# Kernel tuning notes

Hardware: AMD Instinct MI355X
Metric: run time of the kernel (lower is better)

## Reference

```python
import jax, jax.numpy as jnp
import numpy as np
import math

EMBED_DIM = 512
NUM_HEADS = 8
NUM_EXPERTS = 16
TOP_K = 8
B, T = 2, 1024


def setup_inputs() -> dict:
    key = jax.random.key(0)
    ks = jax.random.split(key, 16)
    d, E = EMBED_DIM, NUM_EXPERTS
    hdim = 4 * d  # expert hidden width
    s = 0.02
    inp = {
        "x": jax.random.normal(ks[0], (B, T, d), jnp.float32),
        # RMSNorm params (init ones, matching torch module)
        "g": jnp.ones((d,), jnp.float32),
        "b": jnp.ones((d,), jnp.float32),
        # attention
        "c_attn_w": jax.random.normal(ks[1], (d, 3 * d), jnp.float32) * s,
        "c_attn_b": jnp.zeros((3 * d,), jnp.float32),
        "alpha": jnp.ones((NUM_HEADS,), jnp.float32),
        "c_proj_w": jax.random.normal(ks[2], (d, d), jnp.float32) * s,
        "c_proj_b": jnp.zeros((d,), jnp.float32),
        # router
        "router_w": jax.random.normal(ks[3], (d, E), jnp.float32) * s,
        "router_b": jnp.zeros((E,), jnp.float32),
        # stacked expert params: Linear(d,4d) -> SwiGLU(4d,4d) -> Linear(4d,d)
        "w_in": jax.random.normal(ks[4], (E, d, hdim), jnp.float32) * s,
        "b_in": jnp.zeros((E, hdim), jnp.float32),
        "w1": jax.random.normal(ks[5], (E, hdim, 2 * hdim), jnp.float32) * s,
        "b1": jnp.zeros((E, 2 * hdim), jnp.float32),
        "w2": jax.random.normal(ks[6], (E, hdim, hdim), jnp.float32) * s,
        "b2": jnp.zeros((E, hdim), jnp.float32),
        "w_out": jax.random.normal(ks[7], (E, hdim, d), jnp.float32) * s,
        "b_out": jnp.zeros((E, d), jnp.float32),
    }
    return inp


def _block(x, g, b, c_attn_w, c_attn_b, alpha, c_proj_w, c_proj_b,
           router_w, router_b, w_in, b_in, w1, b1, w2, b2, w_out, b_out):
    Bb, Tt, C = x.shape
    H = alpha.shape[0]
    hd = C // H
    E = router_b.shape[0]

    # RMSNorm (note: additive b, per original module)
    rms = jnp.sqrt(jnp.mean(x * x, axis=-1, keepdims=True) + 1e-6)
    xn = (x / rms) * g + b

    # QK-normalized causal attention
    qkv = xn @ c_attn_w + c_attn_b                      # [B,T,3C]
    q, k, v = jnp.split(qkv, 3, axis=-1)
    def heads(t):
        return t.reshape(Bb, Tt, H, hd).transpose(0, 2, 1, 3)  # [B,H,T,hd]
    q, k, v = heads(q), heads(k), heads(v)
    eps = 1e-5
    q_hat = q / (jnp.linalg.norm(q, axis=-1, keepdims=True) + eps)
    k_hat = k / (jnp.linalg.norm(k, axis=-1, keepdims=True) + eps)
    factor = (alpha * math.sqrt(hd)).reshape(1, H, 1, 1)
    q_scaled = q_hat * factor
    # SDPA default scale = 1/sqrt(head_dim)
    scores = jnp.einsum("bhqd,bhkd->bhqk", q_scaled, k_hat) / math.sqrt(hd)
    causal = jnp.tril(jnp.ones((Tt, Tt), bool))
    scores = jnp.where(causal, scores, -jnp.inf)
    att = jax.nn.softmax(scores, axis=-1)
    y = jnp.einsum("bhqk,bhkd->bhqd", att, v)
    y = y.transpose(0, 2, 1, 3).reshape(Bb, Tt, C)
    y = y @ c_proj_w + c_proj_b
    x = x + y

    # Router + top-8 normalized gates
    routes = jax.nn.softmax(x @ router_w + router_b, axis=-1)  # [B,T,E]
    probs, idx = jax.lax.top_k(routes, TOP_K)
    probs = probs / jnp.sum(probs, axis=-1, keepdims=True)
    # combine weights per expert: [B,T,E]
    gates = jnp.sum(jax.nn.one_hot(idx, E, dtype=x.dtype) * probs[..., None], axis=2)

    # Dense expert evaluation (faithful math: unselected tokens get zero gate)
    N = Bb * Tt
    xf = x.reshape(N, C)
    gf = gates.reshape(N, E)
    h = jnp.einsum("nd,edf->enf", xf, w_in) + b_in[:, None, :]      # [E,N,4d]
    c = jnp.einsum("enf,efg->eng", h, w1) + b1[:, None, :]          # [E,N,8d]
    a, bb2 = jnp.split(c, 2, axis=-1)
    s = (bb2 * jax.nn.sigmoid(bb2)) * a                              # SwiGLU
    o = jnp.einsum("enf,efg->eng", s, w2) + b2[:, None, :]          # [E,N,4d]
    eo = jnp.einsum("enf,efd->end", o, w_out) + b_out[:, None, :]   # [E,N,d]
    moe = jnp.einsum("end,ne->nd", eo, gf).reshape(Bb, Tt, C)
    return x + moe


def reference(x, g, b, c_attn_w, c_attn_b, alpha, c_proj_w, c_proj_b,
              router_w, router_b, w_in, b_in, w1, b1, w2, b2, w_out, b_out):
    return _block(x, g, b, c_attn_w, c_attn_b, alpha, c_proj_w, c_proj_b,
                  router_w, router_b, w_in, b_in, w1, b1, w2, b2, w_out, b_out)
```

## Files before the change

kernel.cpp:

```cpp
#include <hip/hip_runtime.h>
#include <stdint.h>

#define DEVI __device__ __forceinline__
#define FENCE() asm volatile("" ::: "memory")
#define BAR() do{ FENCE(); __builtin_amdgcn_s_barrier(); FENCE(); }while(0)

typedef short short8 __attribute__((ext_vector_type(8)));
typedef short short4v __attribute__((ext_vector_type(4)));
typedef float f32x4 __attribute__((ext_vector_type(4)));

DEVI float bf2f(unsigned short s){ union{unsigned u; float f;} x; x.u = ((unsigned)s)<<16; return x.f; }
DEVI unsigned short f2bf(float f){ union{float f; unsigned u;} x; x.f=f; unsigned r = x.u + 0x7fff + ((x.u>>16)&1); return (unsigned short)(r>>16); }

DEVI void gload_lds16(const void* g, void* l){
  __builtin_amdgcn_global_load_lds((const __attribute__((address_space(1))) unsigned int*)g,
                                   (__attribute__((address_space(3))) unsigned int*)l, 16, 0, 0);
}

__global__ __launch_bounds__(256)
void transpose_cvt(const float* __restrict__ in, unsigned short* __restrict__ out, int K, int N)
{
  __shared__ float tile[32][33];
  size_t zoff = (size_t)blockIdx.z * K * N;
  const float* src = in + zoff;
  unsigned short* dst = out + zoff;
  int kb = blockIdx.y*32, nb = blockIdx.x*32;
  int t = threadIdx.x;
  int tr = t>>3, tc = (t&7)*4;
  float4 v = *(const float4*)(src + (size_t)(kb+tr)*N + nb + tc);
  tile[tr][tc+0]=v.x; tile[tr][tc+1]=v.y; tile[tr][tc+2]=v.z; tile[tr][tc+3]=v.w;
  __syncthreads();
  short4v ov;
  ov[0] = (short)f2bf(tile[tc+0][tr]);
  ov[1] = (short)f2bf(tile[tc+1][tr]);
  ov[2] = (short)f2bf(tile[tc+2][tr]);
  ov[3] = (short)f2bf(tile[tc+3][tr]);
  *(short4v*)(dst + (size_t)(nb+tr)*K + kb + tc) = ov;
}

__global__ __launch_bounds__(256)
void transpose_cvt_w1(const float* __restrict__ w1, unsigned short* __restrict__ outp)
{
  __shared__ float tile[32][33];
  int e = blockIdx.z;
  const float* src = w1 + (size_t)e*2048*4096;
  unsigned short* dst = outp + (size_t)e*4096*2048;
  int np0 = blockIdx.x*32;
  int k0 = blockIdx.y*32;
  int g = np0 >> 5;
  int t = threadIdx.x;
  int tr = t>>3, tc = (t&7)*4;
  int srccol = (tc < 16) ? (g*16 + tc) : (2048 + g*16 + (tc-16));
  float4 v = *(const float4*)(src + (size_t)(k0+tr)*4096 + srccol);
  tile[tr][tc+0]=v.x; tile[tr][tc+1]=v.y; tile[tr][tc+2]=v.z; tile[tr][tc+3]=v.w;
  __syncthreads();
  short4v ov;
  ov[0] = (short)f2bf(tile[tc+0][tr]);
  ov[1] = (short)f2bf(tile[tc+1][tr]);
  ov[2] = (short)f2bf(tile[tc+2][tr]);
  ov[3] = (short)f2bf(tile[tc+3][tr]);
  *(short4v*)(dst + (size_t)(np0+tr)*2048 + k0 + tc) = ov;
}

__global__ __launch_bounds__(256)
void rmsnorm_k(const float* __restrict__ x, const float* __restrict__ gw,
               const float* __restrict__ bw, unsigned short* __restrict__ xn)
{
  int row = blockIdx.x*4 + (threadIdx.x>>6);
  int lane = threadIdx.x & 63;
  const float* xr = x + (size_t)row*512 + lane*8;
  float4 a = *(const float4*)xr;
  float4 c = *(const float4*)(xr+4);
  float ss = a.x*a.x+a.y*a.y+a.z*a.z+a.w*a.w + c.x*c.x+c.y*c.y+c.z*c.z+c.w*c.w;
  #pragma unroll
  for (int m=1;m<64;m<<=1) ss += __shfl_xor(ss, m);
  float inv = 1.0f / sqrtf(ss*(1.f/512.f) + 1e-6f);
  const float* gr = gw + lane*8; const float* br = bw + lane*8;
  float4 g0=*(const float4*)gr, g1=*(const float4*)(gr+4);
  float4 b0=*(const float4*)br, b1=*(const float4*)(br+4);
  short8 o;
  o[0]=(short)f2bf(a.x*inv*g0.x + b0.x);
  o[1]=(short)f2bf(a.y*inv*g0.y + b0.y);
  o[2]=(short)f2bf(a.z*inv*g0.z + b0.z);
  o[3]=(short)f2bf(a.w*inv*g0.w + b0.w);
  o[4]=(short)f2bf(c.x*inv*g1.x + b1.x);
  o[5]=(short)f2bf(c.y*inv*g1.y + b1.y);
  o[6]=(short)f2bf(c.z*inv*g1.z + b1.z);
  o[7]=(short)f2bf(c.w*inv*g1.w + b1.w);
  *(short8*)(xn + (size_t)row*512 + lane*8) = o;
}

#define READ_AFR(Q) do{ \
  _Pragma("unroll") \
  for (int m2=0;m2<2;m2++){ \
    int rt = wm*128 + ((Q)*2+m2)*16 + lrow; \
    _Pragma("unroll") \
    for (int kk=0;kk<2;kk++) \
      afr[m2][kk] = *(const short8*)(sA + rt*128 + (((lg+kk*4)^(rt&7))<<4)); \
  } \
}while(0)

#define QUADP(Q) do{ \
  __builtin_amdgcn_s_setprio(1); \
  _Pragma("unroll") \
  for (int m2=0;m2<2;m2++){ \
    _Pragma("unroll") \
    for (int n=0;n<4;n++){ \
      _Pragma("unroll") \
      for (int kk=0;kk<2;kk++) \
        acc[(Q)*2+m2][n] = __builtin_amdgcn_mfma_f32_16x16x32_bf16(afr[m2][kk], bfr[n][kk], acc[(Q)*2+m2][n], 0,0,0); \
    } \
  } \
  __builtin_amdgcn_s_setprio(0); \
}while(0)

template<int EPI>
__global__ __launch_bounds__(512, 2)
void gemmT(const unsigned short* __restrict__ A, const unsigned short* __restrict__ B,
           const float* __restrict__ bias,
           float* __restrict__ Cf, unsigned short* __restrict__ Ch,
           int M, int N, int K,
           const int* __restrict__ off, long long strideBz, long long strideBiasz)
{
  __shared__ char smem[131072];
  int z = blockIdx.z;
  int rowbase = 0, Mz = M;
  if (off){ rowbase = off[z]; Mz = off[z+1] - rowbase; }
  int row0 = blockIdx.y * 256;
  if (row0 >= Mz) return;
  int col0 = blockIdx.x * 256;
  const unsigned short* Ab = A + (size_t)(rowbase + row0) * K;
  const unsigned short* Bb = B + (size_t)z * strideBz + (size_t)col0 * K;
  const float* biasz = bias + (size_t)z * strideBiasz;

  int tid = threadIdx.x;
  int lane = tid & 63, w = tid >> 6;
  int lrow = lane & 15, lg = lane >> 4;
  int wm = w >> 2, wn = w & 3;

  f32x4 acc[8][4];
  #pragma unroll
  for (int i=0;i<8;i++){
    #pragma unroll
    for (int j=0;j<4;j++) acc[i][j] = f32x4{0.f,0.f,0.f,0.f};
  }
  int nkt = K >> 6;
  auto stage = [&](int kt2, int H){
    if (kt2 >= nkt) return;
    char* sl = smem + (kt2 & 1) * 65536 + H * 16384;
    int k0 = kt2 << 6;
    const unsigned short* src = (H < 2) ? Ab : Bb;
    int rbase = (H & 1) * 128;
    #pragma unroll
    for (int i=0;i<2;i++){
      int si = i*512 + tid;
      int r = si >> 3, kb = (si & 7) ^ (r & 7);
      gload_lds16(src + (size_t)(rbase + r)*K + k0 + kb*8, sl + si*16);
    }
  };
  stage(0,0); stage(0,1); stage(0,2); stage(0,3);
  stage(1,2); stage(1,3);
  asm volatile("s_waitcnt vmcnt(4)" ::: "memory");
  BAR();
  for (int kt = 0; kt < nkt; kt++){
    char* sA = smem + (kt & 1) * 65536;
    char* sB = sA + 32768;
    short8 bfr[4][2], afr[2][2];
    #pragma unroll
    for (int n=0;n<4;n++){
      int ct = wn*64 + n*16 + lrow;
      #pragma unroll
      for (int kk=0;kk<2;kk++)
        bfr[n][kk] = *(const short8*)(sB + ct*128 + (((lg+kk*4)^(ct&7))<<4));
    }
    READ_AFR(0);
    stage(kt+1, 0); stage(kt+1, 1);
    BAR();
    QUADP(0);
    BAR();
    READ_AFR(1);
    stage(kt+2, 2);
    BAR();
    QUADP(1);
    BAR();
    READ_AFR(2);
    stage(kt+2, 3);
    BAR();
    QUADP(2);
    BAR();
    READ_AFR(3);
    if (kt + 2 < nkt) { asm volatile("s_waitcnt vmcnt(4)" ::: "memory"); }
    else              { asm volatile("s_waitcnt vmcnt(0)" ::: "memory"); }
    BAR();
    QUADP(3);
    BAR();
  }
  #pragma unroll
  for (int m=0;m<8;m++){
    #pragma unroll
    for (int j=0;j<4;j++){
      int row = row0 + wm*128 + m*16 + lg*4 + j;
      if (row < Mz){
        size_t rg = (size_t)(rowbase + row);
        if constexpr (EPI == 2){
          #pragma unroll
          for (int nf=0;nf<4;nf+=2){
            int pcol = col0 + wn*64 + nf*16;
            int scol = ((pcol>>5)<<4) + lrow;
            float av = acc[m][nf][j]   + biasz[scol];
            float gv = acc[m][nf+1][j] + biasz[2048 + scol];
            float sg = gv / (1.f + __expf(-gv));
            Ch[rg*2048 + scol] = f2bf(av * sg);
          }
        } else {
          #pragma unroll
          for (int n=0;n<4;n++){
            int col = col0 + wn*64 + n*16 + lrow;
            float v = acc[m][n][j] + biasz[col];
            size_t idx = rg * N + col;
            if constexpr (EPI == 0) Cf[idx] = v;
            else                    Ch[idx] = f2bf(v);
          }
        }
      }
    }
  }
}

__global__ __launch_bounds__(256)
void gemm_proj(const unsigned short* __restrict__ A, const unsigned short* __restrict__ B,
               const float* __restrict__ bias,
               float* __restrict__ Cf, unsigned short* __restrict__ Ch,
               const float* __restrict__ resid, int M, int N, int K)
{
  __shared__ char smem[32768];
  char* smA = smem; char* smB = smem + 16384;
  int row0 = blockIdx.y * 128;
  int col0 = blockIdx.x * 128;
  int t = threadIdx.x, w = t>>6, lane = t&63;
  int lrow = lane&15, lg = lane>>4;
  int wr = w>>1, wc = w&1;

  f32x4 acc[4][4];
  #pragma unroll
  for (int i=0;i<4;i++){
    #pragma unroll
    for (int j=0;j<4;j++) acc[i][j] = f32x4{0.f,0.f,0.f,0.f};
  }
  const size_t Abase = (size_t)row0 * K;
  const size_t Bbase = (size_t)col0 * K;
  int nkt = K >> 6;
  for (int kt=0; kt<nkt; kt++){
    __syncthreads();
    int k0 = kt*64;
    #pragma unroll
    for (int i=0;i<4;i++){
      int s = (i*4 + w)*64 + lane;
      int r = s>>3;
      int kb = (s&7) ^ (r&7);
      gload_lds16(A + Abase + (size_t)r*K + k0 + kb*8, smA + (size_t)(i*4+w)*1024);
      gload_lds16(B + Bbase + (size_t)r*K + k0 + kb*8, smB + (size_t)(i*4+w)*1024);
    }
    __syncthreads();
    #pragma unroll
    for (int ks=0; ks<2; ks++){
      short8 af[4], bf[4];
      int kbb = lg + ks*4;
      #pragma unroll
      for (int m=0;m<4;m++){
        int rt = wr*64 + m*16 + lrow;
        af[m] = *(const short8*)(smA + rt*128 + ((kbb ^ (rt&7))<<4));
      }
      #pragma unroll
      for (int n=0;n<4;n++){
        int rt = wc*64 + n*16 + lrow;
        bf[n] = *(const short8*)(smB + rt*128 + ((kbb ^ (rt&7))<<4));
      }
      #pragma unroll
      for (int m=0;m<4;m++){
        #pragma unroll
        for (int n=0;n<4;n++)
          acc[m][n] = __builtin_amdgcn_mfma_f32_16x16x32_bf16(af[m], bf[n], acc[m][n], 0,0,0);
      }
    }
  }
  #pragma unroll
  for (int m=0;m<4;m++){
    int rloc = wr*64 + m*16 + lg*4;
    #pragma unroll
    for (int j=0;j<4;j++){
      int row = row0 + rloc + j;
      size_t rg = (size_t)row;
      #pragma unroll
      for (int n=0;n<4;n++){
        int col = col0 + wc*64 + n*16 + lrow;
        float v = acc[m][n][j] + bias[col];
        size_t idx = rg * N + col;
        v += resid[idx];
        Cf[idx] = v;
        Ch[idx] = f2bf(v);
      }
    }
  }
}

__global__ __launch_bounds__(256)
void prep_qkv(const float* __restrict__ qkv, const float* __restrict__ alpha,
              unsigned short* __restrict__ q_s, unsigned short* __restrict__ k_hat,
              unsigned short* __restrict__ v_t)
{
  int idx = blockIdx.x*4 + (threadIdx.x>>6);
  int lane = threadIdx.x & 63;
  int h = idx & 7, bt = idx >> 3;
  size_t base = (size_t)bt*1536 + h*64 + lane;
  float qv = qkv[base], kv = qkv[base+512], vv = qkv[base+1024];
  float qs2 = qv*qv, ks2 = kv*kv;
  #pragma unroll
  for (int m=1;m<64;m<<=1){ qs2 += __shfl_xor(qs2, m); ks2 += __shfl_xor(ks2, m); }
  float qh = qv / (sqrtf(qs2) + 1e-5f) * alpha[h];
  float kh = kv / (sqrtf(ks2) + 1e-5f);
  int b = bt >> 10, tt = bt & 1023;
  size_t hb = ((size_t)(b*8+h))*1024*64;
  q_s[hb + (size_t)tt*64 + lane] = f2bf(qh);
  k_hat[hb + (size_t)tt*64 + lane] = f2bf(kh);
  v_t[((size_t)(b*8+h)*64 + lane)*1024 + tt] = f2bf(vv);
}

__global__ __launch_bounds__(256)
void attn_k(const unsigned short* __restrict__ q_s, const unsigned short* __restrict__ k_hat,
            const unsigned short* __restrict__ v_t, unsigned short* __restrict__ y)
{
  __shared__ char sm[51200];
  char* smK = sm + 18432;
  char* smV = sm + 34816;
  int qt = blockIdx.x, bh = blockIdx.y;
  int b = bh>>3, h = bh&7;
  int t = threadIdx.x, w = t>>6, lane = t&63;
  int lrow = lane&15, lg = lane>>4;
  int q0 = qt*64;
  const size_t hQK = (size_t)bh*1024*64;
  const size_t hV  = (size_t)bh*64*1024;

  #pragma unroll
  for (int i=0;i<2;i++){
    int si = i*256 + t;
    int r = si>>3, kb = (si&7)^(r&7);
    gload_lds16(q_s + hQK + (size_t)(q0+r)*64 + kb*8, sm + (size_t)si*16);
  }
  __syncthreads();
  short8 qf[2];
  #pragma unroll
  for (int ks=0;ks<2;ks++){
    int rt = w*16 + lrow;
    int kbb = lg + ks*4;
    qf[ks] = *(const short8*)(sm + rt*128 + ((kbb^(rt&7))<<4));
  }
  f32x4 oacc[4];
  #pragma unroll
  for (int j=0;j<4;j++) oacc[j] = f32x4{0.f,0.f,0.f,0.f};
  float mrun[4], lrun[4];
  #pragma unroll
  for (int j=0;j<4;j++){ mrun[j] = -1e30f; lrun[j] = 0.f; }
  char* Pw = sm + w*2304;

  int ktmax = (q0 + 63) >> 7;
  for (int kt=0; kt<=ktmax; kt++){
    __syncthreads();
    int t0 = kt*128;
    #pragma unroll
    for (int i=0;i<4;i++){
      int s = (i*4+w)*64 + lane;
      int r = s>>3, kb = (s&7)^(r&7);
      gload_lds16(k_hat + hQK + (size_t)(t0+r)*64 + kb*8, smK + (size_t)(i*4+w)*1024);
    }
    #pragma unroll
    for (int i=0;i<4;i++){
      int s = (i*4+w)*64 + lane;
      int d = s>>4, kb2 = s&15;
      int kb = kb2 ^ (d&7);
      gload_lds16(v_t + hV + (size_t)d*1024 + t0 + kb*8, smV + (size_t)(i*4+w)*1024);
    }
    __syncthreads();

    f32x4 sacc[8];
    #pragma unroll
    for (int j=0;j<8;j++) sacc[j] = f32x4{0.f,0.f,0.f,0.f};
    #pragma unroll
    for (int ks=0;ks<2;ks++){
      short8 kf[8];
      int kbb = lg + ks*4;
      #pragma unroll
      for (int nf=0;nf<8;nf++){
        int rt = nf*16+lrow;
        kf[nf] = *(const short8*)(smK + rt*128 + ((kbb^(rt&7))<<4));
      }
      #pragma unroll
      for (int nf=0;nf<8;nf++)
        sacc[nf] = __builtin_amdgcn_mfma_f32_16x16x32_bf16(qf[ks], kf[nf], sacc[nf], 0,0,0);
    }
    if (kt == ktmax){
      #pragma unroll
      for (int nf=0;nf<8;nf++){
        #pragma unroll
        for (int j=0;j<4;j++){
          int qi = q0 + w*16 + lg*4 + j;
          int ki = t0 + nf*16 + lrow;
          if (ki > qi) sacc[nf][j] = -1e30f;
        }
      }
    }
    #pragma unroll
    for (int j=0;j<4;j++){
      float mx = sacc[0][j];
      #pragma unroll
      for (int nf=1;nf<8;nf++) mx = fmaxf(mx, sacc[nf][j]);
      #pragma unroll
      for (int m=1;m<16;m<<=1) mx = fmaxf(mx, __shfl_xor(mx, m));
      float mnew = fmaxf(mrun[j], mx);
      float sc = __expf(mrun[j] - mnew);
      float rs = 0.f;
      #pragma unroll
      for (int nf=0;nf<8;nf++){
        float p = __expf(sacc[nf][j] - mnew);
        sacc[nf][j] = p; rs += p;
      }
      #pragma unroll
      for (int m=1;m<16;m<<=1) rs += __shfl_xor(rs, m);
      lrun[j] = lrun[j]*sc + rs;
      mrun[j] = mnew;
      #pragma unroll
      for (int n2=0;n2<4;n2++) oacc[n2][j] *= sc;
    }
    #pragma unroll
    for (int half=0; half<2; half++){
      #pragma unroll
      for (int nfh=0;nfh<4;nfh++){
        int nf = half*4 + nfh;
        #pragma unroll
        for (int j=0;j<4;j++){
          int row = lg*4 + j;
          int col = nfh*16 + lrow;
          *(unsigned short*)(Pw + (row*72 + col)*2) = f2bf(sacc[nf][j]);
        }
      }
      #pragma unroll
      for (int k2=0;k2<2;k2++){
        int ks2 = half*2 + k2;
        short8 pf, vf[4];
        pf = *(const short8*)(Pw + lrow*144 + lg*16 + k2*64);
        #pragma unroll
        for (int n2=0;n2<4;n2++){
          int d = n2*16+lrow;
          int kbb2 = lg + ks2*4;
          vf[n2] = *(const short8*)(smV + d*256 + ((kbb2^(d&7))<<4));
        }
        #pragma unroll
        for (int n2=0;n2<4;n2++)
          oacc[n2] = __builtin_amdgcn_mfma_f32_16x16x32_bf16(pf, vf[n2], oacc[n2], 0,0,0);
      }
    }
  }
  #pragma unroll
  for (int n2=0;n2<4;n2++){
    #pragma unroll
    for (int j=0;j<4;j++){
      float v = oacc[n2][j] / lrun[j];
      int qi = q0 + w*16 + lg*4 + j;
      int d = n2*16 + lrow;
      y[((size_t)(b*1024+qi))*512 + h*64 + d] = f2bf(v);
    }
  }
}

__global__ __launch_bounds__(256)
void router_topk(const float* __restrict__ x2f, const float* __restrict__ rw,
                 const float* __restrict__ rb, float* __restrict__ gates)
{
  int tkn = blockIdx.x*4 + (threadIdx.x>>6);
  int lane = threadIdx.x & 63;
  int e = lane & 15, p = lane >> 4;
  const float* xr = x2f + (size_t)tkn*512;
  float part = 0.f;
  for (int d = p*128; d < p*128+128; d++)
    part += xr[d] * rw[d*16 + e];
  part += __shfl_xor(part, 16);
  part += __shfl_xor(part, 32);
  float logit = part + rb[e];
  float mx = logit;
  #pragma unroll
  for (int m=1;m<16;m<<=1) mx = fmaxf(mx, __shfl_xor(mx, m));
  float ex = __expf(logit - mx);
  float sm = ex;
  #pragma unroll
  for (int m=1;m<16;m<<=1) sm += __shfl_xor(sm, m);
  float prob = ex / sm;
  bool taken = false;
  float ssum = 0.f;
  #pragma unroll
  for (int r=0;r<8;r++){
    float cv = taken ? -1.f : prob;
    int ci = e;
    #pragma unroll
    for (int m=1;m<16;m<<=1){
      float ov = __shfl_xor(cv, m);
      int oi = __shfl_xor(ci, m);
      if (ov > cv || (ov == cv && oi < ci)){ cv = ov; ci = oi; }
    }
    if (e == ci) taken = true;
    ssum += cv;
  }
  if (lane < 16)
    gates[(size_t)tkn*16 + e] = taken ? prob / ssum : 0.f;
}

__global__ void listbuild(const float* __restrict__ gates, int* __restrict__ list,
                          int* __restrict__ slot, int* __restrict__ cnt)
{
  int e = blockIdx.x;
  int tid = threadIdx.x, w = tid>>6, lane = tid&63;
  __shared__ int sbase;
  __shared__ int wsum[4];
  if (tid==0) sbase = 0;
  __syncthreads();
  for (int c=0;c<8;c++){
    int tk = c*256 + tid;
    bool flag = gates[(size_t)tk*16 + e] > 0.f;
    unsigned long long bal = __ballot(flag);
    if (lane==0) wsum[w] = (int)__popcll(bal);
    __syncthreads();
    int wpref = 0;
    for (int i=0;i<w;i++) wpref += wsum[i];
    int tot = wsum[0]+wsum[1]+wsum[2]+wsum[3];
    int lpref = (int)__popcll(bal & ((1ull<<lane)-1ull));
    if (flag){
      int pos = sbase + wpref + lpref;
      list[e*2048 + pos] = tk;
      slot[(size_t)tk*16 + e] = pos;
    }
    __syncthreads();
    if (tid==0) sbase += tot;
    __syncthreads();
  }
  if (tid==0) cnt[e] = sbase;
}

__global__ void prefix_off(const int* __restrict__ cnt, int* __restrict__ off){
  if (threadIdx.x==0 && blockIdx.x==0){
    int a=0;
    for (int e=0;e<16;e++){ off[e]=a; a+=cnt[e]; }
    off[16]=a;
  }
}

__global__ __launch_bounds__(256)
void gather_rows(const unsigned short* __restrict__ x2h, const int* __restrict__ list,
                 const int* __restrict__ cnt, const int* __restrict__ off,
                 unsigned short* __restrict__ xe)
{
  int e = blockIdx.y;
  int s = blockIdx.x*4 + (threadIdx.x>>6);
  if (s >= cnt[e]) return;
  int lane = threadIdx.x & 63;
  int tk = list[e*2048 + s];
  *(short8*)(xe + ((size_t)(off[e]+s))*512 + lane*8) =
      *(const short8*)(x2h + (size_t)tk*512 + lane*8);
}

__global__ __launch_bounds__(256)
void combine_k(const float* __restrict__ x2f, const unsigned short* __restrict__ eo,
               const float* __restrict__ gates, const int* __restrict__ slot,
               const int* __restrict__ off, float* __restrict__ out)
{
  int tkn = blockIdx.x;
  __shared__ float gs[16];
  __shared__ int rws[16];
  int tid = threadIdx.x;
  if (tid < 16){
    float g = gates[(size_t)tkn*16 + tid];
    gs[tid] = g;
    rws[tid] = (g > 0.f) ? (off[tid] + slot[(size_t)tkn*16 + tid]) : 0;
  }
  __syncthreads();
  for (int d = tid; d < 512; d += 256){
    float v = x2f[(size_t)tkn*512 + d];
    #pragma unroll
    for (int e=0;e<16;e++){
      float g = gs[e];
      if (g > 0.f) v += g * bf2f(eo[(size_t)rws[e]*512 + d]);
    }
    out[(size_t)tkn*512 + d] = v;
  }
}

extern "C" void kernel_launch(void* const* d_in, const int* in_sizes, int n_in,
                              void* d_out, int out_size, void* d_ws, size_t ws_size,
                              hipStream_t stream) {
  (void)in_sizes; (void)n_in; (void)out_size; (void)ws_size;
  const float* x    = (const float*)d_in[0];
  const float* gw   = (const float*)d_in[1];
  const float* bw   = (const float*)d_in[2];
  const float* caw  = (const float*)d_in[3];
  const float* cab  = (const float*)d_in[4];
  const float* alpha= (const float*)d_in[5];
  const float* cpw  = (const float*)d_in[6];
  const float* cpb  = (const float*)d_in[7];
  const float* rw   = (const float*)d_in[8];
  const float* rb   = (const float*)d_in[9];
  const float* w_in = (const float*)d_in[10];
  const float* b_in = (const float*)d_in[11];
  const float* w1   = (const float*)d_in[12];
  const float* b1   = (const float*)d_in[13];
  const float* w2   = (const float*)d_in[14];
  const float* b2   = (const float*)d_in[15];
  const float* w_out= (const float*)d_in[16];
  const float* b_out= (const float*)d_in[17];

  char* ws = (char*)d_ws;
  size_t o = 0;
  auto alloc = [&](size_t bytes)->char*{
    char* p = ws + o;
    o += (bytes + 255) & ~(size_t)255;
    return p;
  };
  const size_t PADROWS = 16896;
  unsigned short* wT_attn = (unsigned short*)alloc(1536ull*512*2);
  unsigned short* wT_proj = (unsigned short*)alloc(512ull*512*2);
  unsigned short* wT_in   = (unsigned short*)alloc(16ull*2048*512*2);
  unsigned short* wT1p    = (unsigned short*)alloc(16ull*4096*2048*2);
  unsigned short* wT_2    = (unsigned short*)alloc(16ull*2048*2048*2);
  unsigned short* wT_out  = (unsigned short*)alloc(16ull*512*2048*2);
  unsigned short* xn      = (unsigned short*)alloc(2048ull*512*2);
  float*          qkv     = (float*)alloc(2048ull*1536*4);
  unsigned short* q_s     = (unsigned short*)alloc(2048ull*512*2);
  unsigned short* k_hat   = (unsigned short*)alloc(2048ull*512*2);
  unsigned short* v_t     = (unsigned short*)alloc(2048ull*512*2);
  unsigned short* ybuf    = (unsigned short*)alloc(2048ull*512*2);
  float*          x2f     = (float*)alloc(2048ull*512*4);
  unsigned short* x2h     = (unsigned short*)alloc(2048ull*512*2);
  float*          gates   = (float*)alloc(2048ull*16*4);
  int*            slot    = (int*)alloc(2048ull*16*4);
  int*            list    = (int*)alloc(16ull*2048*4);
  int*            cnt     = (int*)alloc(64);
  int*            off     = (int*)alloc(256);
  unsigned short* xe      = (unsigned short*)alloc(PADROWS*512*2);
  unsigned short* hbuf    = (unsigned short*)alloc(PADROWS*2048*2);
  unsigned short* sbuf    = (unsigned short*)alloc(PADROWS*2048*2);
  unsigned short* eobuf   = xe;
  unsigned short* obuf    = hbuf;

  dim3 blk(256);
  dim3 blk5(512);
  transpose_cvt<<<dim3(1536/32, 512/32, 1), blk, 0, stream>>>(caw, wT_attn, 512, 1536);
  transpose_cvt<<<dim3(512/32, 512/32, 1), blk, 0, stream>>>(cpw, wT_proj, 512, 512);
  transpose_cvt<<<dim3(2048/32, 512/32, 16), blk, 0, stream>>>(w_in, wT_in, 512, 2048);
  transpose_cvt_w1<<<dim3(4096/32, 2048/32, 16), blk, 0, stream>>>(w1, wT1p);
  transpose_cvt<<<dim3(2048/32, 2048/32, 16), blk, 0, stream>>>(w2, wT_2, 2048, 2048);
  transpose_cvt<<<dim3(512/32, 2048/32, 16), blk, 0, stream>>>(w_out, wT_out, 2048, 512);

  rmsnorm_k<<<512, blk, 0, stream>>>(x, gw, bw, xn);
  gemmT<0><<<dim3(6, 8, 1), blk5, 0, stream>>>(xn, wT_attn, cab, qkv, nullptr,
                                               2048, 1536, 512, nullptr, 0, 0);
  prep_qkv<<<4096, blk, 0, stream>>>(qkv, alpha, q_s, k_hat, v_t);
  attn_k<<<dim3(16,16), blk, 0, stream>>>(q_s, k_hat, v_t, ybuf);
  gemm_proj<<<dim3(4,16,1), blk, 0, stream>>>(ybuf, wT_proj, cpb, x2f, x2h, x, 2048, 512, 512);
  router_topk<<<512, blk, 0, stream>>>(x2f, rw, rb, gates);
  listbuild<<<16, blk, 0, stream>>>(gates, list, slot, cnt);
  prefix_off<<<1, 64, 0, stream>>>(cnt, off);
  gather_rows<<<dim3(512,16), blk, 0, stream>>>(x2h, list, cnt, off, xe);

  gemmT<1><<<dim3(8,8,16), blk5, 0, stream>>>(xe, wT_in, b_in, nullptr, hbuf,
                                              0, 2048, 512, off, 2048ll*512, 2048);
  gemmT<2><<<dim3(16,8,16), blk5, 0, stream>>>(hbuf, wT1p, b1, nullptr, sbuf,
                                               0, 4096, 2048, off, 4096ll*2048, 4096);
  gemmT<1><<<dim3(8,8,16), blk5, 0, stream>>>(sbuf, wT_2, b2, nullptr, obuf,
                                              0, 2048, 2048, off, 2048ll*2048, 2048);
  gemmT<1><<<dim3(2,8,16), blk5, 0, stream>>>(obuf, wT_out, b_out, nullptr, eobuf,
                                              0, 512, 2048, off, 512ll*2048, 512);
  combine_k<<<2048, blk, 0, stream>>>(x2f, eobuf, gates, slot, off, (float*)d_out);
}
```

Before: 1.105 ms.

## Merge weight transposes with RMSNorm; fuse QK-norm and head split into QKV GEMM epilogue

```diff
diff --git a/kernel.cpp b/kernel.cpp
--- a/kernel.cpp
+++ b/kernel.cpp
@@ -17,15 +17,9 @@
                                    (__attribute__((address_space(3))) unsigned int*)l, 16, 0, 0);
 }
 
-__global__ __launch_bounds__(256)
-void transpose_cvt(const float* __restrict__ in, unsigned short* __restrict__ out, int K, int N)
-{
-  __shared__ float tile[32][33];
-  size_t zoff = (size_t)blockIdx.z * K * N;
-  const float* src = in + zoff;
-  unsigned short* dst = out + zoff;
-  int kb = blockIdx.y*32, nb = blockIdx.x*32;
-  int t = threadIdx.x;
+DEVI void tr_tile(const float* __restrict__ src, unsigned short* __restrict__ dst,
+                  int K, int N, int kb, int nb, int t, float (*tile)[33])
+{
   int tr = t>>3, tc = (t&7)*4;
   float4 v = *(const float4*)(src + (size_t)(kb+tr)*N + nb + tc);
   tile[tr][tc+0]=v.x; tile[tr][tc+1]=v.y; tile[tr][tc+2]=v.z; tile[tr][tc+3]=v.w;
@@ -39,55 +33,93 @@
 }
 
 __global__ __launch_bounds__(256)
-void transpose_cvt_w1(const float* __restrict__ w1, unsigned short* __restrict__ outp)
+void prep_all(const float* __restrict__ caw, const float* __restrict__ cpw,
+              const float* __restrict__ w_in, const float* __restrict__ w1,
+              const float* __restrict__ w2, const float* __restrict__ w_out,
+              unsigned short* __restrict__ wT_attn, unsigned short* __restrict__ wT_proj,
+              unsigned short* __restrict__ wT_in, unsigned short* __restrict__ wT1p,
+              unsigned short* __restrict__ wT_2, unsigned short* __restrict__ wT_out,
+              const float* __restrict__ x, const float* __restrict__ gw,
+              const float* __restrict__ bw, unsigned short* __restrict__ xn)
 {
   __shared__ float tile[32][33];
-  int e = blockIdx.z;
-  const float* src = w1 + (size_t)e*2048*4096;
-  unsigned short* dst = outp + (size_t)e*4096*2048;
-  int np0 = blockIdx.x*32;
-  int k0 = blockIdx.y*32;
-  int g = np0 >> 5;
+  int bid = blockIdx.x;
   int t = threadIdx.x;
-  int tr = t>>3, tc = (t&7)*4;
-  int srccol = (tc < 16) ? (g*16 + tc) : (2048 + g*16 + (tc-16));
-  float4 v = *(const float4*)(src + (size_t)(k0+tr)*4096 + srccol);
-  tile[tr][tc+0]=v.x; tile[tr][tc+1]=v.y; tile[tr][tc+2]=v.z; tile[tr][tc+3]=v.w;
-  __syncthreads();
-  short4v ov;
-  ov[0] = (short)f2bf(tile[tc+0][tr]);
-  ov[1] = (short)f2bf(tile[tc+1][tr]);
-  ov[2] = (short)f2bf(tile[tc+2][tr]);
-  ov[3] = (short)f2bf(tile[tc+3][tr]);
-  *(short4v*)(dst + (size_t)(np0+tr)*2048 + k0 + tc) = ov;
-}
-
-__global__ __launch_bounds__(256)
-void rmsnorm_k(const float* __restrict__ x, const float* __restrict__ gw,
-               const float* __restrict__ bw, unsigned short* __restrict__ xn)
-{
-  int row = blockIdx.x*4 + (threadIdx.x>>6);
-  int lane = threadIdx.x & 63;
-  const float* xr = x + (size_t)row*512 + lane*8;
-  float4 a = *(const float4*)xr;
-  float4 c = *(const float4*)(xr+4);
-  float ss = a.x*a.x+a.y*a.y+a.z*a.z+a.w*a.w + c.x*c.x+c.y*c.y+c.z*c.z+c.w*c.w;
-  #pragma unroll
-  for (int m=1;m<64;m<<=1) ss += __shfl_xor(ss, m);
-  float inv = 1.0f / sqrtf(ss*(1.f/512.f) + 1e-6f);
-  const float* gr = gw + lane*8; const float* br = bw + lane*8;
-  float4 g0=*(const float4*)gr, g1=*(const float4*)(gr+4);
-  float4 b0=*(const float4*)br, b1=*(const float4*)(br+4);
-  short8 o;
-  o[0]=(short)f2bf(a.x*inv*g0.x + b0.x);
-  o[1]=(short)f2bf(a.y*inv*g0.y + b0.y);
-  o[2]=(short)f2bf(a.z*inv*g0.z + b0.z);
-  o[3]=(short)f2bf(a.w*inv*g0.w + b0.w);
-  o[4]=(short)f2bf(c.x*inv*g1.x + b1.x);
-  o[5]=(short)f2bf(c.y*inv*g1.y + b1.y);
-  o[6]=(short)f2bf(c.z*inv*g1.z + b1.z);
-  o[7]=(short)f2bf(c.w*inv*g1.w + b1.w);
-  *(short8*)(xn + (size_t)row*512 + lane*8) = o;
+  if (bid < 768){
+    int xb = bid % 48, yb = bid / 48;
+    tr_tile(caw, wT_attn, 512, 1536, yb*32, xb*32, t, tile); return;
+  }
+  bid -= 768;
+  if (bid < 256){
+    int xb = bid % 16, yb = bid / 16;
+    tr_tile(cpw, wT_proj, 512, 512, yb*32, xb*32, t, tile); return;
+  }
+  bid -= 256;
+  if (bid < 16384){
+    int z = bid >> 10, r = bid & 1023;
+    int xb = r % 64, yb = r / 64;
+    tr_tile(w_in + (size_t)z*512*2048, wT_in + (size_t)z*2048*512,
+            512, 2048, yb*32, xb*32, t, tile); return;
+  }
+  bid -= 16384;
+  if (bid < 131072){
+    int z = bid >> 13, r = bid & 8191;
+    int xb = r % 128, yb = r / 128;
+    const float* src = w1 + (size_t)z*2048*4096;
+    unsigned short* dst = wT1p + (size_t)z*4096*2048;
+    int np0 = xb*32, k0 = yb*32, g = np0 >> 5;
+    int trr = t>>3, tc = (t&7)*4;
+    int srccol = (tc < 16) ? (g*16 + tc) : (2048 + g*16 + (tc-16));
+    float4 v = *(const float4*)(src + (size_t)(k0+trr)*4096 + srccol);
+    tile[trr][tc+0]=v.x; tile[trr][tc+1]=v.y; tile[trr][tc+2]=v.z; tile[trr][tc+3]=v.w;
+    __syncthreads();
+    short4v ov;
+    ov[0] = (short)f2bf(tile[tc+0][trr]);
+    ov[1] = (short)f2bf(tile[tc+1][trr]);
+    ov[2] = (short)f2bf(tile[tc+2][trr]);
+    ov[3] = (short)f2bf(tile[tc+3][trr]);
+    *(short4v*)(dst + (size_t)(np0+trr)*2048 + k0 + tc) = ov;
+    return;
+  }
+  bid -= 131072;
+  if (bid < 65536){
+    int z = bid >> 12, r = bid & 4095;
+    int xb = r % 64, yb = r / 64;
+    tr_tile(w2 + (size_t)z*2048*2048, wT_2 + (size_t)z*2048*2048,
+            2048, 2048, yb*32, xb*32, t, tile); return;
+  }
+  bid -= 65536;
+  if (bid < 16384){
+    int z = bid >> 10, r = bid & 1023;
+    int xb = r % 16, yb = r / 16;
+    tr_tile(w_out + (size_t)z*2048*512, wT_out + (size_t)z*512*2048,
+            2048, 512, yb*32, xb*32, t, tile); return;
+  }
+  bid -= 16384;
+  {
+    int row = bid*4 + (t>>6);
+    int lane = t & 63;
+    const float* xr = x + (size_t)row*512 + lane*8;
+    float4 a = *(const float4*)xr;
+    float4 c = *(const float4*)(xr+4);
+    float ss = a.x*a.x+a.y*a.y+a.z*a.z+a.w*a.w + c.x*c.x+c.y*c.y+c.z*c.z+c.w*c.w;
+    #pragma unroll
+    for (int m=1;m<64;m<<=1) ss += __shfl_xor(ss, m);
+    float inv = 1.0f / sqrtf(ss*(1.f/512.f) + 1e-6f);
+    const float* gr = gw + lane*8; const float* br = bw + lane*8;
+    float4 g0=*(const float4*)gr, g1=*(const float4*)(gr+4);
+    float4 b0=*(const float4*)br, b1=*(const float4*)(br+4);
+    short8 o;
+    o[0]=(short)f2bf(a.x*inv*g0.x + b0.x);
+    o[1]=(short)f2bf(a.y*inv*g0.y + b0.y);
+    o[2]=(short)f2bf(a.z*inv*g0.z + b0.z);
+    o[3]=(short)f2bf(a.w*inv*g0.w + b0.w);
+    o[4]=(short)f2bf(c.x*inv*g1.x + b1.x);
+    o[5]=(short)f2bf(c.y*inv*g1.y + b1.y);
+    o[6]=(short)f2bf(c.z*inv*g1.z + b1.z);
+    o[7]=(short)f2bf(c.w*inv*g1.w + b1.w);
+    *(short8*)(xn + (size_t)row*512 + lane*8) = o;
+  }
 }
 
 #define READ_AFR(Q) do{ \
@@ -120,7 +152,9 @@
            const float* __restrict__ bias,
            float* __restrict__ Cf, unsigned short* __restrict__ Ch,
            int M, int N, int K,
-           const int* __restrict__ off, long long strideBz, long long strideBiasz)
+           const int* __restrict__ off, long long strideBz, long long strideBiasz,
+           const float* __restrict__ alpha, unsigned short* __restrict__ oq,
+           unsigned short* __restrict__ ok, unsigned short* __restrict__ ov)
 {
   __shared__ char smem[131072];
   int z = blockIdx.z;
@@ -195,31 +229,71 @@
     QUADP(3);
     BAR();
   }
-  #pragma unroll
-  for (int m=0;m<8;m++){
-    #pragma unroll
-    for (int j=0;j<4;j++){
-      int row = row0 + wm*128 + m*16 + lg*4 + j;
-      if (row < Mz){
-        size_t rg = (size_t)(rowbase + row);
-        if constexpr (EPI == 2){
+  if constexpr (EPI == 3){
+    int tcol = col0 + wn*64;
+    int type = tcol >> 9;
+    int hd = (tcol >> 6) & 7;
+    float al = alpha[hd];
+    #pragma unroll
+    for (int m=0;m<8;m++){
+      #pragma unroll
+      for (int j=0;j<4;j++){
+        int row = row0 + wm*128 + m*16 + lg*4 + j;
+        float v4[4]; float ss = 0.f;
+        #pragma unroll
+        for (int n=0;n<4;n++){
+          int col = tcol + n*16 + lrow;
+          v4[n] = acc[m][n][j] + biasz[col];
+          ss += v4[n]*v4[n];
+        }
+        ss += __shfl_xor(ss,1); ss += __shfl_xor(ss,2);
+        ss += __shfl_xor(ss,4); ss += __shfl_xor(ss,8);
+        int b = row >> 10, tt = row & 1023;
+        size_t hb = ((size_t)(b*8+hd))*65536;
+        if (type == 0){
+          float sc = al / (sqrtf(ss) + 1e-5f);
           #pragma unroll
-          for (int nf=0;nf<4;nf+=2){
-            int pcol = col0 + wn*64 + nf*16;
-            int scol = ((pcol>>5)<<4) + lrow;
-            float av = acc[m][nf][j]   + biasz[scol];
-            float gv = acc[m][nf+1][j] + biasz[2048 + scol];
-            float sg = gv / (1.f + __expf(-gv));
-            Ch[rg*2048 + scol] = f2bf(av * sg);
-          }
+          for (int n=0;n<4;n++)
+            oq[hb + (size_t)tt*64 + n*16 + lrow] = f2bf(v4[n]*sc);
+        } else if (type == 1){
+          float sc = 1.f / (sqrtf(ss) + 1e-5f);
+          #pragma unroll
+          for (int n=0;n<4;n++)
+            ok[hb + (size_t)tt*64 + n*16 + lrow] = f2bf(v4[n]*sc);
         } else {
           #pragma unroll
-          for (int n=0;n<4;n++){
-            int col = col0 + wn*64 + n*16 + lrow;
-            float v = acc[m][n][j] + biasz[col];
-            size_t idx = rg * N + col;
-            if constexpr (EPI == 0) Cf[idx] = v;
-            else                    Ch[idx] = f2bf(v);
+          for (int n=0;n<4;n++)
+            ov[((size_t)(b*8+hd)*64 + n*16 + lrow)*1024 + tt] = f2bf(v4[n]);
+        }
+      }
+    }
+  } else {
+    #pragma unroll
+    for (int m=0;m<8;m++){
+      #pragma unroll
+      for (int j=0;j<4;j++){
+        int row = row0 + wm*128 + m*16 + lg*4 + j;
+        if (row < Mz){
+          size_t rg = (size_t)(rowbase + row);
+          if constexpr (EPI == 2){
+            #pragma unroll
+            for (int nf=0;nf<4;nf+=2){
+              int pcol = col0 + wn*64 + nf*16;
+              int scol = ((pcol>>5)<<4) + lrow;
+              float av = acc[m][nf][j]   + biasz[scol];
+              float gv = acc[m][nf+1][j] + biasz[2048 + scol];
+              float sg = gv / (1.f + __expf(-gv));
+              Ch[rg*2048 + scol] = f2bf(av * sg);
+            }
+          } else {
+            #pragma unroll
+            for (int n=0;n<4;n++){
+              int col = col0 + wn*64 + n*16 + lrow;
+              float v = acc[m][n][j] + biasz[col];
+              size_t idx = rg * N + col;
+              if constexpr (EPI == 0) Cf[idx] = v;
+              else                    Ch[idx] = f2bf(v);
+            }
           }
         }
       }
@@ -302,28 +376,6 @@
       }
     }
   }
-}
-
-__global__ __launch_bounds__(256)
-void prep_qkv(const float* __restrict__ qkv, const float* __restrict__ alpha,
-              unsigned short* __restrict__ q_s, unsigned short* __restrict__ k_hat,
-              unsigned short* __restrict__ v_t)
-{
-  int idx = blockIdx.x*4 + (threadIdx.x>>6);
-  int lane = threadIdx.x & 63;
-  int h = idx & 7, bt = idx >> 3;
-  size_t base = (size_t)bt*1536 + h*64 + lane;
-  float qv = qkv[base], kv = qkv[base+512], vv = qkv[base+1024];
-  float qs2 = qv*qv, ks2 = kv*kv;
-  #pragma unroll
-  for (int m=1;m<64;m<<=1){ qs2 += __shfl_xor(qs2, m); ks2 += __shfl_xor(ks2, m); }
-  float qh = qv / (sqrtf(qs2) + 1e-5f) * alpha[h];
-  float kh = kv / (sqrtf(ks2) + 1e-5f);
-  int b = bt >> 10, tt = bt & 1023;
-  size_t hb = ((size_t)(b*8+h))*1024*64;
-  q_s[hb + (size_t)tt*64 + lane] = f2bf(qh);
-  k_hat[hb + (size_t)tt*64 + lane] = f2bf(kh);
-  v_t[((size_t)(b*8+h)*64 + lane)*1024 + tt] = f2bf(vv);
 }
 
 __global__ __launch_bounds__(256)
@@ -630,7 +682,6 @@
   unsigned short* wT_2    = (unsigned short*)alloc(16ull*2048*2048*2);
   unsigned short* wT_out  = (unsigned short*)alloc(16ull*512*2048*2);
   unsigned short* xn      = (unsigned short*)alloc(2048ull*512*2);
-  float*          qkv     = (float*)alloc(2048ull*1536*4);
   unsigned short* q_s     = (unsigned short*)alloc(2048ull*512*2);
   unsigned short* k_hat   = (unsigned short*)alloc(2048ull*512*2);
   unsigned short* v_t     = (unsigned short*)alloc(2048ull*512*2);
@@ -650,17 +701,13 @@
 
   dim3 blk(256);
   dim3 blk5(512);
-  transpose_cvt<<<dim3(1536/32, 512/32, 1), blk, 0, stream>>>(caw, wT_attn, 512, 1536);
-  transpose_cvt<<<dim3(512/32, 512/32, 1), blk, 0, stream>>>(cpw, wT_proj, 512, 512);
-  transpose_cvt<<<dim3(2048/32, 512/32, 16), blk, 0, stream>>>(w_in, wT_in, 512, 2048);
-  transpose_cvt_w1<<<dim3(4096/32, 2048/32, 16), blk, 0, stream>>>(w1, wT1p);
-  transpose_cvt<<<dim3(2048/32, 2048/32, 16), blk, 0, stream>>>(w2, wT_2, 2048, 2048);
-  transpose_cvt<<<dim3(512/32, 2048/32, 16), blk, 0, stream>>>(w_out, wT_out, 2048, 512);
-
-  rmsnorm_k<<<512, blk, 0, stream>>>(x, gw, bw, xn);
-  gemmT<0><<<dim3(6, 8, 1), blk5, 0, stream>>>(xn, wT_attn, cab, qkv, nullptr,
-                                               2048, 1536, 512, nullptr, 0, 0);
-  prep_qkv<<<4096, blk, 0, stream>>>(qkv, alpha, q_s, k_hat, v_t);
+  prep_all<<<230912, blk, 0, stream>>>(caw, cpw, w_in, w1, w2, w_out,
+                                       wT_attn, wT_proj, wT_in, wT1p, wT_2, wT_out,
+                                       x, gw, bw, xn);
+
+  gemmT<3><<<dim3(6, 8, 1), blk5, 0, stream>>>(xn, wT_attn, cab, nullptr, nullptr,
+                                               2048, 1536, 512, nullptr, 0, 0,
+                                               alpha, q_s, k_hat, v_t);
   attn_k<<<dim3(16,16), blk, 0, stream>>>(q_s, k_hat, v_t, ybuf);
   gemm_proj<<<dim3(4,16,1), blk, 0, stream>>>(ybuf, wT_proj, cpb, x2f, x2h, x, 2048, 512, 512);
   router_topk<<<512, blk, 0, stream>>>(x2f, rw, rb, gates);
@@ -669,12 +716,16 @@
   gather_rows<<<dim3(512,16), blk, 0, stream>>>(x2h, list, cnt, off, xe);
 
   gemmT<1><<<dim3(8,8,16), blk5, 0, stream>>>(xe, wT_in, b_in, nullptr, hbuf,
-                                              0, 2048, 512, off, 2048ll*512, 2048);
+                                              0, 2048, 512, off, 2048ll*512, 2048,
+                                              nullptr, nullptr, nullptr, nullptr);
   gemmT<2><<<dim3(16,8,16), blk5, 0, stream>>>(hbuf, wT1p, b1, nullptr, sbuf,
-                                               0, 4096, 2048, off, 4096ll*2048, 4096);
+                                               0, 4096, 2048, off, 4096ll*2048, 4096,
+                                               nullptr, nullptr, nullptr, nullptr);
   gemmT<1><<<dim3(8,8,16), blk5, 0, stream>>>(sbuf, wT_2, b2, nullptr, obuf,
-                                              0, 2048, 2048, off, 2048ll*2048, 2048);
+                                              0, 2048, 2048, off, 2048ll*2048, 2048,
+                                              nullptr, nullptr, nullptr, nullptr);
   gemmT<1><<<dim3(2,8,16), blk5, 0, stream>>>(obuf, wT_out, b_out, nullptr, eobuf,
-                                              0, 512, 2048, off, 512ll*2048, 512);
+                                              0, 512, 2048, off, 512ll*2048, 512,
+                                              nullptr, nullptr, nullptr, nullptr);
   combine_k<<<2048, blk, 0, stream>>>(x2f, eobuf, gates, slot, off, (float*)d_out);
 }
```

Measured after the change: 1.094 ms. About the same (-1.0%).
